# Optimization experiments

Measured on AMD Instinct MI355X. Metric: run time of the kernel, lower is better.

Reference implementation:

```python
import jax, jax.numpy as jnp
import numpy as np

N_HEAD = 16
BLOCK_SIZE = 2049  # w2 last dim = block_size - 1 = 2048


def setup_inputs() -> dict:
    key = jax.random.key(0)
    ks = jax.random.split(key, 9)
    B, T, C = 2, 2048, 1024
    hd = C // N_HEAD
    M = BLOCK_SIZE - 1
    return {
        "x": jax.random.normal(ks[0], (B, T, C), jnp.float32),
        "w1_w": jax.random.normal(ks[1], (C, C), jnp.float32) * 0.02,
        "w1_b": jax.random.normal(ks[2], (C,), jnp.float32) * 0.02,
        # torch uniform_(a=-0.001, b=0.001)
        "w2": jax.random.uniform(ks[3], (N_HEAD, hd, M), jnp.float32, -0.001, 0.001),
        "b2": jax.random.normal(ks[4], (M,), jnp.float32) * 0.02,
        "value_w": jax.random.normal(ks[5], (C, C), jnp.float32) * 0.02,
        "value_b": jax.random.normal(ks[6], (C,), jnp.float32) * 0.02,
        "proj_w": jax.random.normal(ks[7], (C, C), jnp.float32) * 0.02,
        "proj_b": jax.random.normal(ks[8], (C,), jnp.float32) * 0.02,
    }


def reference(x, w1_w, w1_b, w2, b2, value_w, value_b, proj_w, proj_b):
    B, T, C = x.shape
    H = N_HEAD
    hd = C // H
    M = w2.shape[-1]  # block_size - 1
    # kernel = relu(w1(x)), split heads -> [B, H, T, hd]
    k = jax.nn.relu(x @ w1_w.T + w1_b).reshape(B, T, H, hd).transpose(0, 2, 1, 3)
    # synthesizer scores: [B, H, T, M]
    attn = jnp.einsum('bhtd,hdm->bhtm', k, w2) + b2
    # causal mask = tril(ones(block,block))[:T, :M] == 0 -> -inf
    causal = jnp.tril(jnp.ones((T, M), dtype=bool))
    attn = jnp.where(causal, attn, -jnp.inf)
    # softmax over first T score columns
    attn = jax.nn.softmax(attn[..., :T], axis=-1)  # [B, H, T, T]
    v = (x @ value_w.T + value_b).reshape(B, T, H, hd).transpose(0, 2, 1, 3)
    out = jnp.einsum('bhts,bhsd->bhtd', attn, v)
    out = out.transpose(0, 2, 1, 3).reshape(B, T, C)
    return out @ proj_w.T + proj_b
```

## Files before the change

### kernel.cpp

```cpp
#include <hip/hip_runtime.h>
#include <math.h>
#include <stdint.h>

typedef __bf16 bf16;
typedef __bf16 bf16x8 __attribute__((ext_vector_type(8)));
typedef __bf16 bf16x4 __attribute__((ext_vector_type(4)));
typedef float f32x4 __attribute__((ext_vector_type(4)));
typedef unsigned int u32;

__device__ __forceinline__ int swz(int row, int chunk) {
    return row * 64 + ((chunk ^ (row & 7)) << 3);
}

__device__ __forceinline__ void gld16(void* lds, const void* g) {
    __builtin_amdgcn_global_load_lds(
        (const __attribute__((address_space(1))) u32*)g,
        (__attribute__((address_space(3))) u32*)lds, 16, 0, 0);
}

__device__ __forceinline__ void stage64(bf16* dst, const bf16* src, size_t srcStride,
                                        int w, int l) {
    #pragma unroll
    for (int i = 0; i < 2; ++i) {
        const int br = (w * 2 + i) * 8;
        const int r = br + (l >> 3);
        const int gs = (l & 7) ^ (r & 7);
        gld16(dst + br * 64, src + (size_t)r * srcStride + gs * 8);
    }
}

__global__ void cast_bf16_k(const float* __restrict__ src, bf16* __restrict__ dst, int n) {
    const int stride = gridDim.x * blockDim.x * 4;
    for (int i = (blockIdx.x * blockDim.x + threadIdx.x) * 4; i < n; i += stride) {
        float4 v = *(const float4*)(src + i);
        bf16x4 o = {(bf16)v.x, (bf16)v.y, (bf16)v.z, (bf16)v.w};
        *(bf16x4*)(dst + i) = o;
    }
}

__global__ __launch_bounds__(256) void w2_transpose_k(const float* __restrict__ w2,
                                                      bf16* __restrict__ w2t, int M) {
    __shared__ float Tf[64][65];
    const int h = blockIdx.y, m0 = blockIdx.x * 64, t = threadIdx.x;
    {
        const int dr = t >> 4, c4 = (t & 15) * 4;
        #pragma unroll
        for (int it = 0; it < 4; ++it) {
            const int d = dr + it * 16;
            float4 v = *(const float4*)(w2 + ((size_t)h * 64 + d) * M + m0 + c4);
            Tf[d][c4] = v.x; Tf[d][c4 + 1] = v.y; Tf[d][c4 + 2] = v.z; Tf[d][c4 + 3] = v.w;
        }
    }
    __syncthreads();
    const int m = t >> 2;
    #pragma unroll
    for (int it = 0; it < 2; ++it) {
        const int ch = (t & 3) + it * 4;
        bf16x8 o;
        #pragma unroll
        for (int j = 0; j < 8; ++j) o[j] = (bf16)Tf[ch * 8 + j][m];
        *(bf16x8*)(w2t + ((size_t)h * M + m0 + m) * 64 + ch * 8) = o;
    }
}

__global__ __launch_bounds__(256) void gemm_bf16_k(const bf16* __restrict__ A,
                                                   const bf16* __restrict__ Bw,
                                                   const float* __restrict__ bias,
                                                   const float* __restrict__ bias2,
                                                   float* __restrict__ C0,
                                                   bf16* __restrict__ CK,
                                                   bf16* __restrict__ CV,
                                                   int M, int N, int K, int mode, int Ns)
{
    __shared__ __align__(16) bf16 As[128 * 64];
    __shared__ __align__(16) bf16 Bs[128 * 64];
    const int tid = threadIdx.x;
    const int w = tid >> 6, l = tid & 63;
    const int wr = w >> 1, wc = w & 1;
    const int lc = l & 15, lg = l >> 4;
    const int row0 = blockIdx.y * 128, col0 = blockIdx.x * 128;

    f32x4 acc[4][4] = {};

    for (int k0 = 0; k0 < K; k0 += 64) {
        __syncthreads();
        #pragma unroll
        for (int i = 0; i < 4; ++i) {
            const int br = (w * 4 + i) * 8;
            const int r = br + (l >> 3);
            const int gs = (l & 7) ^ (r & 7);
            gld16(As + br * 64, A  + (size_t)(row0 + r) * K + k0 + gs * 8);
            gld16(Bs + br * 64, Bw + (size_t)(col0 + r) * K + k0 + gs * 8);
        }
        __syncthreads();
        #pragma unroll
        for (int ks = 0; ks < 2; ++ks) {
            bf16x8 af[4], bfv[4];
            #pragma unroll
            for (int i = 0; i < 4; ++i) {
                af[i]  = *(const bf16x8*)&As[swz(wr * 64 + i * 16 + lc, ks * 4 + lg)];
                bfv[i] = *(const bf16x8*)&Bs[swz(wc * 64 + i * 16 + lc, ks * 4 + lg)];
            }
            #pragma unroll
            for (int mi = 0; mi < 4; ++mi)
                #pragma unroll
                for (int ni = 0; ni < 4; ++ni)
                    acc[mi][ni] = __builtin_amdgcn_mfma_f32_16x16x32_bf16(af[mi], bfv[ni], acc[mi][ni], 0, 0, 0);
        }
    }

    #pragma unroll
    for (int ni = 0; ni < 4; ++ni) {
        const int col = col0 + wc * 64 + ni * 16 + lc;
        #pragma unroll
        for (int mi = 0; mi < 4; ++mi) {
            const int rowb = row0 + wr * 64 + mi * 16 + lg * 4;
            f32x4 v = acc[mi][ni];
            if (mode == 0) {
                const float bv = bias[col];
                #pragma unroll
                for (int r = 0; r < 4; ++r)
                    C0[(size_t)(rowb + r) * N + col] = v[r] + bv;
            } else if (col < Ns) {
                const float bv = bias[col];
                #pragma unroll
                for (int r = 0; r < 4; ++r)
                    CK[(size_t)(rowb + r) * Ns + col] = (bf16)fmaxf(v[r] + bv, 0.f);
            } else {
                const float bv = bias2[col - Ns];
                const int b = rowb >> 11, tt = rowb & 2047;
                bf16x4 o = {(bf16)(v[0] + bv), (bf16)(v[1] + bv),
                            (bf16)(v[2] + bv), (bf16)(v[3] + bv)};
                *(bf16x4*)(CV + ((size_t)b * Ns + (col - Ns)) * 2048 + tt) = o;
            }
        }
    }
}

__global__ __launch_bounds__(256, 2) void synth_attn_v6(const bf16* __restrict__ Kb,
                                                        const bf16* __restrict__ VT,
                                                        const bf16* __restrict__ w2t,
                                                        const float* __restrict__ b2,
                                                        bf16* __restrict__ Ob)
{
    constexpr int T = 2048, C = 1024, M = 2048;
    __shared__ __align__(16) bf16 Wl[2][64 * 64];
    __shared__ __align__(16) bf16 Vl[2][64 * 64];
    __shared__ __align__(16) bf16 Pl[4][16 * 64];
    const int tid = threadIdx.x;
    const int w = tid >> 6, l = tid & 63;
    const int lc = l & 15, lg = l >> 4;

    const int bx = blockIdx.x;
    const int pr = bx & 15, hb = bx >> 4;
    const int h = hb & 15, b = hb >> 4;

    const bf16* Wgt = w2t + (size_t)h * M * 64;
    const bf16* Vgt = VT + ((size_t)b * C + h * 64) * T;
    bf16* Pw = &Pl[w][0];

    #pragma unroll 1
    for (int half = 0; half < 2; ++half) {
        const int tb = half ? (31 - pr) : pr;
        const int t0 = tb * 64;

        const bf16* Kg = Kb + (size_t)(b * T + t0 + w * 16 + lc) * C + h * 64;
        const bf16x8 kf0 = *(const bf16x8*)(Kg + lg * 8);
        const bf16x8 kf1 = *(const bf16x8*)(Kg + 32 + lg * 8);

        f32x4 acc[4] = {};
        float lsum[4] = {0.f, 0.f, 0.f, 0.f};

        stage64(&Wl[0][0], Wgt, 64, w, l);
        stage64(&Vl[0][0], Vgt, T, w, l);
        __syncthreads();

        for (int sb = 0; sb <= tb; ++sb) {
            const int cur = sb & 1;
            const int s0 = sb * 64;

            f32x4 sv[4];
            #pragma unroll
            for (int st = 0; st < 4; ++st) {
                const float bb = b2[s0 + st * 16 + lc];
                sv[st] = {bb, bb, bb, bb};
            }
            if (sb < tb) {
                stage64(&Wl[cur ^ 1][0], Wgt + (size_t)(s0 + 64) * 64, 64, w, l);
                stage64(&Vl[cur ^ 1][0], Vgt + (s0 + 64), T, w, l);
            }

            #pragma unroll
            for (int st = 0; st < 4; ++st) {
                bf16x8 wb0 = *(const bf16x8*)&Wl[cur][swz(st * 16 + lc, lg)];
                bf16x8 wb1 = *(const bf16x8*)&Wl[cur][swz(st * 16 + lc, 4 + lg)];
                sv[st] = __builtin_amdgcn_mfma_f32_16x16x32_bf16(kf0, wb0, sv[st], 0, 0, 0);
                sv[st] = __builtin_amdgcn_mfma_f32_16x16x32_bf16(kf1, wb1, sv[st], 0, 0, 0);
            }

            const bool diag = (sb == tb);
            #pragma unroll
            for (int st = 0; st < 4; ++st) {
                const int scol = st * 16 + lc;
                #pragma unroll
                for (int r = 0; r < 4; ++r) {
                    float e = __expf(sv[st][r]);
                    if (diag && scol > w * 16 + lg * 4 + r) e = 0.f;
                    lsum[r] += e;
                    const int trow = lg * 4 + r;
                    Pw[trow * 64 + (((scol >> 3) ^ (trow & 7)) << 3) + (scol & 7)] = (bf16)e;
                }
            }

            #pragma unroll
            for (int ks = 0; ks < 2; ++ks) {
                bf16x8 pf = *(const bf16x8*)&Pw[swz(lc, ks * 4 + lg)];
                #pragma unroll
                for (int dt = 0; dt < 4; ++dt) {
                    bf16x8 vv = *(const bf16x8*)&Vl[cur][swz(dt * 16 + lc, ks * 4 + lg)];
                    acc[dt] = __builtin_amdgcn_mfma_f32_16x16x32_bf16(pf, vv, acc[dt], 0, 0, 0);
                }
            }

            __syncthreads();
        }

        #pragma unroll
        for (int r = 0; r < 4; ++r) {
            float ls = lsum[r];
            ls += __shfl_xor(ls, 1);
            ls += __shfl_xor(ls, 2);
            ls += __shfl_xor(ls, 4);
            ls += __shfl_xor(ls, 8);
            const float inv = 1.f / ls;
            bf16* dst = Ob + (size_t)(b * T + t0 + w * 16 + lg * 4 + r) * C + h * 64;
            #pragma unroll
            for (int dt = 0; dt < 4; ++dt)
                dst[dt * 16 + lc] = (bf16)(acc[dt][r] * inv);
        }
    }
}

extern "C" void kernel_launch(void* const* d_in, const int* in_sizes, int n_in,
                              void* d_out, int out_size, void* d_ws, size_t ws_size,
                              hipStream_t stream) {
    const float* x       = (const float*)d_in[0];
    const float* w1_w    = (const float*)d_in[1];
    const float* w1_b    = (const float*)d_in[2];
    const float* w2      = (const float*)d_in[3];
    const float* b2      = (const float*)d_in[4];
    const float* value_w = (const float*)d_in[5];
    const float* value_b = (const float*)d_in[6];
    const float* proj_w  = (const float*)d_in[7];
    const float* proj_b  = (const float*)d_in[8];

    const int B = 2, T = 2048, C = 1024, H = 16, M = 2048;
    const int R = B * T;

    bf16* xb  = (bf16*)d_ws;
    bf16* w1b = xb  + (size_t)R * C;
    bf16* vwb = w1b + (size_t)C * C;
    bf16* w2t = vwb + (size_t)C * C;
    bf16* pwb = w2t + (size_t)H * M * 64;
    bf16* Kb  = pwb + (size_t)C * C;
    bf16* VTb = Kb  + (size_t)R * C;
    bf16* Ob  = VTb + (size_t)R * C;

    cast_bf16_k<<<1024, 256, 0, stream>>>(x, xb, R * C);
    cast_bf16_k<<<256, 256, 0, stream>>>(w1_w, w1b, C * C);
    cast_bf16_k<<<256, 256, 0, stream>>>(value_w, vwb, C * C);
    cast_bf16_k<<<256, 256, 0, stream>>>(proj_w, pwb, C * C);
    w2_transpose_k<<<dim3(M / 64, H), 256, 0, stream>>>(w2, w2t, M);

    gemm_bf16_k<<<dim3(2 * C / 128, R / 128), 256, 0, stream>>>(
        xb, w1b, w1_b, value_b, nullptr, Kb, VTb, R, 2 * C, C, 1, C);

    synth_attn_v6<<<dim3(512), 256, 0, stream>>>(Kb, VTb, w2t, b2, Ob);

    gemm_bf16_k<<<dim3(C / 128, R / 128), 256, 0, stream>>>(
        Ob, pwb, proj_b, nullptr, (float*)d_out, nullptr, nullptr, R, C, C, 0, C);
}
```

Measured before the change: 120.3 us.

## Process paired query tiles together sharing W/V loads with triple-buffered pipeline

Each block now computes its two causal query tiles (j and 31-j) in one pass over the key tiles, instead of one after the other. Each staged W2/V tile is reused for both accumulators, which cuts global-to-LDS traffic and halves the loop prologues. Staging moves to a three-deep buffer with explicit vmcnt waits and a single barrier per step, so loads run further ahead of compute. The cost is more registers for the two accumulator sets and more LDS, which could hurt occupancy or cause spills.

```diff
diff --git a/kernel.cpp b/kernel.cpp
--- a/kernel.cpp
+++ b/kernel.cpp
@@ -137,106 +137,126 @@
     }
 }
 
-__global__ __launch_bounds__(256, 2) void synth_attn_v6(const bf16* __restrict__ Kb,
+__device__ __forceinline__ void tile_step(bf16x8 kf0, bf16x8 kf1,
+                                          const bf16* Wb, const bf16* Vb,
+                                          bf16* Pw, const float (&bb)[4],
+                                          f32x4 (&acc)[4], float (&lsum)[4],
+                                          bool diag, int lc, int lg, int w)
+{
+    f32x4 sv[4];
+    #pragma unroll
+    for (int st = 0; st < 4; ++st) sv[st] = {bb[st], bb[st], bb[st], bb[st]};
+    #pragma unroll
+    for (int st = 0; st < 4; ++st) {
+        bf16x8 wb0 = *(const bf16x8*)&Wb[swz(st * 16 + lc, lg)];
+        bf16x8 wb1 = *(const bf16x8*)&Wb[swz(st * 16 + lc, 4 + lg)];
+        sv[st] = __builtin_amdgcn_mfma_f32_16x16x32_bf16(kf0, wb0, sv[st], 0, 0, 0);
+        sv[st] = __builtin_amdgcn_mfma_f32_16x16x32_bf16(kf1, wb1, sv[st], 0, 0, 0);
+    }
+    #pragma unroll
+    for (int st = 0; st < 4; ++st) {
+        const int scol = st * 16 + lc;
+        #pragma unroll
+        for (int r = 0; r < 4; ++r) {
+            float e = __expf(sv[st][r]);
+            if (diag && scol > w * 16 + lg * 4 + r) e = 0.f;
+            lsum[r] += e;
+            const int trow = lg * 4 + r;
+            Pw[trow * 64 + (((scol >> 3) ^ (trow & 7)) << 3) + (scol & 7)] = (bf16)e;
+        }
+    }
+    #pragma unroll
+    for (int ks = 0; ks < 2; ++ks) {
+        bf16x8 pf = *(const bf16x8*)&Pw[swz(lc, ks * 4 + lg)];
+        #pragma unroll
+        for (int dt = 0; dt < 4; ++dt) {
+            bf16x8 vv = *(const bf16x8*)&Vb[swz(dt * 16 + lc, ks * 4 + lg)];
+            acc[dt] = __builtin_amdgcn_mfma_f32_16x16x32_bf16(pf, vv, acc[dt], 0, 0, 0);
+        }
+    }
+}
+
+__global__ __launch_bounds__(256, 2) void synth_attn_v7(const bf16* __restrict__ Kb,
                                                         const bf16* __restrict__ VT,
                                                         const bf16* __restrict__ w2t,
                                                         const float* __restrict__ b2,
                                                         bf16* __restrict__ Ob)
 {
     constexpr int T = 2048, C = 1024, M = 2048;
-    __shared__ __align__(16) bf16 Wl[2][64 * 64];
-    __shared__ __align__(16) bf16 Vl[2][64 * 64];
+    __shared__ __align__(16) bf16 Wl[3][64 * 64];
+    __shared__ __align__(16) bf16 Vl[3][64 * 64];
     __shared__ __align__(16) bf16 Pl[4][16 * 64];
     const int tid = threadIdx.x;
     const int w = tid >> 6, l = tid & 63;
     const int lc = l & 15, lg = l >> 4;
 
     const int bx = blockIdx.x;
-    const int pr = bx & 15, hb = bx >> 4;
-    const int h = hb & 15, b = hb >> 4;
+    const int half = bx >> 8, idx = bx & 255;
+    const int jj = idx & 15;
+    const int j = half ? (15 - jj) : jj;
+    const int bh = (half << 4) | (idx >> 4);
+    const int h = bh & 15, b = bh >> 4;
+    const int tA = j, tB = 31 - j;
+    const int t0A = tA * 64, t0B = tB * 64;
 
     const bf16* Wgt = w2t + (size_t)h * M * 64;
     const bf16* Vgt = VT + ((size_t)b * C + h * 64) * T;
     bf16* Pw = &Pl[w][0];
 
-    #pragma unroll 1
-    for (int half = 0; half < 2; ++half) {
-        const int tb = half ? (31 - pr) : pr;
-        const int t0 = tb * 64;
-
-        const bf16* Kg = Kb + (size_t)(b * T + t0 + w * 16 + lc) * C + h * 64;
-        const bf16x8 kf0 = *(const bf16x8*)(Kg + lg * 8);
-        const bf16x8 kf1 = *(const bf16x8*)(Kg + 32 + lg * 8);
-
-        f32x4 acc[4] = {};
-        float lsum[4] = {0.f, 0.f, 0.f, 0.f};
-
-        stage64(&Wl[0][0], Wgt, 64, w, l);
-        stage64(&Vl[0][0], Vgt, T, w, l);
-        __syncthreads();
-
-        for (int sb = 0; sb <= tb; ++sb) {
-            const int cur = sb & 1;
-            const int s0 = sb * 64;
-
-            f32x4 sv[4];
-            #pragma unroll
-            for (int st = 0; st < 4; ++st) {
-                const float bb = b2[s0 + st * 16 + lc];
-                sv[st] = {bb, bb, bb, bb};
-            }
-            if (sb < tb) {
-                stage64(&Wl[cur ^ 1][0], Wgt + (size_t)(s0 + 64) * 64, 64, w, l);
-                stage64(&Vl[cur ^ 1][0], Vgt + (s0 + 64), T, w, l);
-            }
-
-            #pragma unroll
-            for (int st = 0; st < 4; ++st) {
-                bf16x8 wb0 = *(const bf16x8*)&Wl[cur][swz(st * 16 + lc, lg)];
-                bf16x8 wb1 = *(const bf16x8*)&Wl[cur][swz(st * 16 + lc, 4 + lg)];
-                sv[st] = __builtin_amdgcn_mfma_f32_16x16x32_bf16(kf0, wb0, sv[st], 0, 0, 0);
-                sv[st] = __builtin_amdgcn_mfma_f32_16x16x32_bf16(kf1, wb1, sv[st], 0, 0, 0);
-            }
-
-            const bool diag = (sb == tb);
-            #pragma unroll
-            for (int st = 0; st < 4; ++st) {
-                const int scol = st * 16 + lc;
-                #pragma unroll
-                for (int r = 0; r < 4; ++r) {
-                    float e = __expf(sv[st][r]);
-                    if (diag && scol > w * 16 + lg * 4 + r) e = 0.f;
-                    lsum[r] += e;
-                    const int trow = lg * 4 + r;
-                    Pw[trow * 64 + (((scol >> 3) ^ (trow & 7)) << 3) + (scol & 7)] = (bf16)e;
-                }
-            }
-
-            #pragma unroll
-            for (int ks = 0; ks < 2; ++ks) {
-                bf16x8 pf = *(const bf16x8*)&Pw[swz(lc, ks * 4 + lg)];
-                #pragma unroll
-                for (int dt = 0; dt < 4; ++dt) {
-                    bf16x8 vv = *(const bf16x8*)&Vl[cur][swz(dt * 16 + lc, ks * 4 + lg)];
-                    acc[dt] = __builtin_amdgcn_mfma_f32_16x16x32_bf16(pf, vv, acc[dt], 0, 0, 0);
-                }
-            }
-
-            __syncthreads();
-        }
-
-        #pragma unroll
-        for (int r = 0; r < 4; ++r) {
-            float ls = lsum[r];
-            ls += __shfl_xor(ls, 1);
-            ls += __shfl_xor(ls, 2);
-            ls += __shfl_xor(ls, 4);
-            ls += __shfl_xor(ls, 8);
-            const float inv = 1.f / ls;
-            bf16* dst = Ob + (size_t)(b * T + t0 + w * 16 + lg * 4 + r) * C + h * 64;
-            #pragma unroll
-            for (int dt = 0; dt < 4; ++dt)
-                dst[dt * 16 + lc] = (bf16)(acc[dt][r] * inv);
+    const bf16* KgA = Kb + (size_t)(b * T + t0A + w * 16 + lc) * C + h * 64;
+    const bf16* KgB = Kb + (size_t)(b * T + t0B + w * 16 + lc) * C + h * 64;
+    const bf16x8 kfA0 = *(const bf16x8*)(KgA + lg * 8);
+    const bf16x8 kfA1 = *(const bf16x8*)(KgA + 32 + lg * 8);
+    const bf16x8 kfB0 = *(const bf16x8*)(KgB + lg * 8);
+    const bf16x8 kfB1 = *(const bf16x8*)(KgB + 32 + lg * 8);
+
+    f32x4 accA[4] = {}, accB[4] = {};
+    float lsA[4] = {0.f, 0.f, 0.f, 0.f}, lsB[4] = {0.f, 0.f, 0.f, 0.f};
+
+    stage64(&Wl[0][0], Wgt, 64, w, l);
+    stage64(&Vl[0][0], Vgt, T, w, l);
+    stage64(&Wl[1][0], Wgt + (size_t)64 * 64, 64, w, l);
+    stage64(&Vl[1][0], Vgt + 64, T, w, l);
+
+    int cur = 0;
+    for (int sb = 0; sb <= tB; ++sb) {
+        const int s0 = sb * 64;
+        if (sb < tB) asm volatile("s_waitcnt vmcnt(4)" ::: "memory");
+        else         asm volatile("s_waitcnt vmcnt(0)" ::: "memory");
+        __builtin_amdgcn_s_barrier();
+
+        float bb[4];
+        #pragma unroll
+        for (int st = 0; st < 4; ++st) bb[st] = b2[s0 + st * 16 + lc];
+
+        tile_step(kfB0, kfB1, &Wl[cur][0], &Vl[cur][0], Pw, bb, accB, lsB,
+                  sb == tB, lc, lg, w);
+        if (sb <= tA)
+            tile_step(kfA0, kfA1, &Wl[cur][0], &Vl[cur][0], Pw, bb, accA, lsA,
+                      sb == tA, lc, lg, w);
+
+        if (sb + 2 <= tB) {
+            int nx = cur + 2; if (nx >= 3) nx -= 3;
+            stage64(&Wl[nx][0], Wgt + (size_t)(s0 + 128) * 64, 64, w, l);
+            stage64(&Vl[nx][0], Vgt + (s0 + 128), T, w, l);
+        }
+        if (++cur == 3) cur = 0;
+    }
+
+    #pragma unroll
+    for (int r = 0; r < 4; ++r) {
+        float la = lsA[r], lb = lsB[r];
+        la += __shfl_xor(la, 1); la += __shfl_xor(la, 2);
+        la += __shfl_xor(la, 4); la += __shfl_xor(la, 8);
+        lb += __shfl_xor(lb, 1); lb += __shfl_xor(lb, 2);
+        lb += __shfl_xor(lb, 4); lb += __shfl_xor(lb, 8);
+        const float ia = 1.f / la, ib = 1.f / lb;
+        bf16* dA = Ob + (size_t)(b * T + t0A + w * 16 + lg * 4 + r) * C + h * 64;
+        bf16* dB = Ob + (size_t)(b * T + t0B + w * 16 + lg * 4 + r) * C + h * 64;
+        #pragma unroll
+        for (int dt = 0; dt < 4; ++dt) {
+            dA[dt * 16 + lc] = (bf16)(accA[dt][r] * ia);
+            dB[dt * 16 + lc] = (bf16)(accB[dt][r] * ib);
         }
     }
 }
@@ -275,7 +295,7 @@
     gemm_bf16_k<<<dim3(2 * C / 128, R / 128), 256, 0, stream>>>(
         xb, w1b, w1_b, value_b, nullptr, Kb, VTb, R, 2 * C, C, 1, C);
 
-    synth_attn_v6<<<dim3(512), 256, 0, stream>>>(Kb, VTb, w2t, b2, Ob);
+    synth_attn_v7<<<dim3(512), 256, 0, stream>>>(Kb, VTb, w2t, b2, Ob);
 
     gemm_bf16_k<<<dim3(C / 128, R / 128), 256, 0, stream>>>(
         Ob, pwb, proj_b, nullptr, (float*)d_out, nullptr, nullptr, R, C, C, 0, C);
```

New measurement: 116.1 us. -3.5%, faster.
